# Performance work log

Hardware: AMD Instinct MI355X
Metric: run time of the kernel (lower is better)

The kernel has to match this reference:

```python
import jax, jax.numpy as jnp
import numpy as np


def setup_inputs() -> dict:
    key = jax.random.key(0)
    k1, k2, k3 = jax.random.split(key, 3)
    B, T, D = 2, 2048, 1024
    x = jax.random.normal(k1, (B, T, D), dtype=jnp.float32)
    w_qkv = jax.random.normal(k2, (3 * D, D), dtype=jnp.float32) * (D ** -0.5)
    w_out = jax.random.normal(k3, (D, D), dtype=jnp.float32) * (D ** -0.5)
    return {"x": x, "w_qkv": w_qkv, "w_out": w_out, "heads": 16}


def reference(x, w_qkv, w_out, heads):
    # SelfAttention forward: attention_type='sdp', position_mode='alibi', causal=True, eval mode.
    B, T, D = x.shape
    H = heads
    hd = D // H
    scale = hd ** -0.5

    # qkv projection: torch Linear -> x @ W^T
    qkv = (x @ w_qkv.T).reshape(B, T, 3, H, hd)
    qkv = jnp.transpose(qkv, (2, 0, 3, 1, 4))  # [3, B, H, T, hd]
    q, k, v = qkv[0], qkv[1], qkv[2]

    # ALiBi relative bias: slopes = 1 / 2^(h/H) for h = 1..H
    slopes = 1.0 / jnp.power(2.0, jnp.arange(1, H + 1, dtype=jnp.float32) / H)
    pos = jnp.arange(T, dtype=jnp.float32)
    rel = jnp.abs(pos[:, None] - pos[None, :])  # [T, T]
    bias = -slopes[None, :, None, None] * rel[None, None, :, :]  # [1, H, T, T]

    # scores + causal mask + softmax (manual path since position_bias is not None)
    scores = jnp.einsum('bhqd,bhkd->bhqk', q, k) * scale + bias
    causal_mask = jnp.triu(jnp.ones((T, T), dtype=bool), k=1)
    scores = jnp.where(causal_mask[None, None, :, :], -jnp.inf, scores)
    attn = jax.nn.softmax(scores, axis=-1)
    attn = jnp.where(jnp.isnan(attn), 1.0 / float(max(T, 1)), attn)

    out = jnp.einsum('bhqk,bhkd->bhqd', attn, v)  # [B, H, T, hd]
    out = jnp.transpose(out, (0, 2, 1, 3)).reshape(B, T, D)
    return out @ w_out.T
```

## Files before the change

kernel.cpp:

```cpp
#include <hip/hip_runtime.h>
#include <hip/hip_bf16.h>

typedef __attribute__((ext_vector_type(8))) short shortx8;
typedef __attribute__((ext_vector_type(4))) float floatx4;
typedef __attribute__((ext_vector_type(16))) float floatx16;
typedef __attribute__((ext_vector_type(4))) unsigned uintx4;
typedef __attribute__((ext_vector_type(2))) unsigned uintx2;

#define B_ 2
#define T_ 2048
#define D_ 1024
#define H_ 16
#define HD_ 64
#define SCALE 0.125f
#define QSCALE 0.18033688011112042f
#define SMAX2 23.083120654223414f
#define FULLH ((size_t)B_ * H_ * T_ * HD_)

#define GLDS16(g, l) __builtin_amdgcn_global_load_lds( \
    (__attribute__((address_space(1))) void*)(g), \
    (__attribute__((address_space(3))) void*)(l), 16, 0, 0)

__device__ __forceinline__ short f2bf(float f) {
    union { float f; unsigned u; } v; v.f = f;
    unsigned r = v.u + 0x7FFFu + ((v.u >> 16) & 1u);
    return (short)(r >> 16);
}

__device__ __forceinline__ unsigned pk2(float x, float y) {
    union { __hip_bfloat162 h; unsigned u; } t;
    t.h = __float22bfloat162_rn(make_float2(x, y));
    return t.u;
}

__device__ __forceinline__ shortx8 cvt8(floatx4 a, floatx4 b) {
    uintx4 r = { pk2(a[0], a[1]), pk2(a[2], a[3]), pk2(b[0], b[1]), pk2(b[2], b[3]) };
    return __builtin_bit_cast(shortx8, r);
}

__device__ __forceinline__ float ex2(float x) {
#if __has_builtin(__builtin_amdgcn_exp2f)
    return __builtin_amdgcn_exp2f(x);
#else
    return exp2f(x);
#endif
}

__global__ __launch_bounds__(256) void cvt_xw(const float* __restrict__ x,
                                              const float* __restrict__ wqkv,
                                              short* __restrict__ xbf,
                                              short* __restrict__ wbf) {
    int i = blockIdx.x * 256 + threadIdx.x;
    const float* src; short* dst; int o;
    if (i < 524288) { src = x; dst = xbf; o = i; }
    else            { src = wqkv; dst = wbf; o = i - 524288; }
    const floatx4* p = reinterpret_cast<const floatx4*>(src) + (size_t)o * 2;
    *(reinterpret_cast<shortx8*>(dst) + o) = cvt8(p[0], p[1]);
}

__global__ __launch_bounds__(256) void qkv_fast(const short* __restrict__ xbf,
                                                const short* __restrict__ wbf,
                                                short* __restrict__ qout,
                                                short* __restrict__ kv) {
    __shared__ __align__(16) short As[128 * 64];
    __shared__ __align__(16) short Bs[128 * 64];

    const int tid = threadIdx.x;
    const int wv = tid >> 6;
    const int l  = tid & 63;
    const int ln = l & 15;
    const int quad = l >> 4;
    const int rowb = quad << 2;
    const int wm = wv >> 1, wn = wv & 1;
    const int m0 = blockIdx.y * 128;
    const int n0g = blockIdx.x * 128;

    const int lr = l >> 3, lc = l & 7;
    const int gcol = (lc ^ lr) << 3;
    const short* agp = xbf + (size_t)(m0 + wv * 32 + lr) * D_ + gcol;
    const short* bgp = wbf + (size_t)(n0g + wv * 32 + lr) * D_ + gcol;
    short* aldsb = As + wv * 32 * 64;
    short* bldsb = Bs + wv * 32 * 64;

    floatx4 acc[4][4] = {};

    for (int k0 = 0; k0 < D_; k0 += 64) {
        __syncthreads();
#pragma unroll
        for (int c = 0; c < 4; ++c) {
            GLDS16(agp + (size_t)(c * 8) * D_ + k0, aldsb + c * 512);
            GLDS16(bgp + (size_t)(c * 8) * D_ + k0, bldsb + c * 512);
        }
        __syncthreads();

#pragma unroll
        for (int kk = 0; kk < 2; ++kk) {
            const int csw = (kk << 2) + quad;
            const int sw = (csw ^ (ln & 7)) << 3;
            shortx8 af[4], bf[4];
#pragma unroll
            for (int i = 0; i < 4; ++i)
                af[i] = *reinterpret_cast<const shortx8*>(&As[((wm * 64 + i * 16 + ln) << 6) + sw]);
#pragma unroll
            for (int j = 0; j < 4; ++j)
                bf[j] = *reinterpret_cast<const shortx8*>(&Bs[((wn * 64 + j * 16 + ln) << 6) + sw]);
#pragma unroll
            for (int i = 0; i < 4; ++i)
#pragma unroll
                for (int j = 0; j < 4; ++j)
                    acc[i][j] = __builtin_amdgcn_mfma_f32_16x16x32_bf16(af[i], bf[j], acc[i][j], 0, 0, 0);
        }
    }

    const int sel = n0g >> 10;
    const int bb = m0 >> 11;
    const int t0w = (m0 + wm * 64) & (T_ - 1);
    const int h = ((n0g + wn * 64) >> 6) & 15;

    if (sel < 2) {
        short* dst = (sel == 0) ? qout : kv;
        const float sc = (sel == 0) ? QSCALE : 1.0f;
        const size_t hb = (size_t)(bb * H_ + h) * T_;
#pragma unroll
        for (int i = 0; i < 4; ++i)
#pragma unroll
            for (int r = 0; r < 4; ++r) {
                int t = t0w + i * 16 + rowb + r;
#pragma unroll
                for (int j = 0; j < 4; ++j)
                    dst[(hb + t) * HD_ + j * 16 + ln] = f2bf(acc[i][j][r] * sc);
            }
    } else {
        __syncthreads();
        short* tb = (wv < 2) ? (As + wv * 4096) : (Bs + (wv - 2) * 4096);
        short* vhead = kv + FULLH + (size_t)(bb * H_ + h) * HD_ * T_;
        const int dl = l & 31, th = (l >> 5) << 5;
#pragma unroll
        for (int p = 0; p < 2; ++p) {
#pragma unroll
            for (int i = 0; i < 4; ++i)
#pragma unroll
                for (int jj = 0; jj < 2; ++jj) {
                    int j = 2 * p + jj;
#pragma unroll
                    for (int r = 0; r < 4; ++r)
                        tb[(jj * 16 + ln) * 72 + i * 16 + rowb + r] = f2bf(acc[i][j][r]);
                }
            short* vd = vhead + (size_t)(p * 32 + dl) * T_ + t0w + th;
#pragma unroll
            for (int seg = 0; seg < 4; ++seg)
                *reinterpret_cast<shortx8*>(vd + seg * 8) =
                    *reinterpret_cast<const shortx8*>(&tb[dl * 72 + th + seg * 8]);
        }
    }
}

__global__ __launch_bounds__(256) void out_fast(const short* __restrict__ Abf,
                                                const short* __restrict__ wbf,
                                                float* __restrict__ out) {
    __shared__ __align__(16) short As[128 * 64];
    __shared__ __align__(16) short Bs[128 * 64];

    const int tid = threadIdx.x;
    const int wv = tid >> 6;
    const int l  = tid & 63;
    const int ln = l & 15;
    const int quad = l >> 4;
    const int rowb = quad << 2;
    const int wm = wv >> 1, wn = wv & 1;
    const int m0 = blockIdx.y * 128;
    const int n0g = blockIdx.x * 128;

    const int lr = l >> 3, lc = l & 7;
    const int gcol = (lc ^ lr) << 3;
    const short* bgp = wbf + (size_t)(n0g + wv * 32 + lr) * D_ + gcol;
    short* aldsb = As + wv * 32 * 64;
    short* bldsb = Bs + wv * 32 * 64;

    size_t abase[4];
#pragma unroll
    for (int c = 0; c < 4; ++c) {
        int m = m0 + wv * 32 + c * 8 + lr;
        int bb2 = m >> 11, t = m & (T_ - 1);
        abase[c] = ((size_t)(bb2 * H_) * T_ + t) * HD_ + gcol;
    }

    floatx4 acc[4][4] = {};

    for (int k0 = 0; k0 < D_; k0 += 64) {
        const size_t hoff = (size_t)(k0 >> 6) * T_ * HD_;
        __syncthreads();
#pragma unroll
        for (int c = 0; c < 4; ++c) {
            GLDS16(Abf + abase[c] + hoff, aldsb + c * 512);
            GLDS16(bgp + (size_t)(c * 8) * D_ + k0, bldsb + c * 512);
        }
        __syncthreads();

#pragma unroll
        for (int kk = 0; kk < 2; ++kk) {
            const int csw = (kk << 2) + quad;
            const int sw = (csw ^ (ln & 7)) << 3;
            shortx8 af[4], bf[4];
#pragma unroll
            for (int i = 0; i < 4; ++i)
                af[i] = *reinterpret_cast<const shortx8*>(&As[((wm * 64 + i * 16 + ln) << 6) + sw]);
#pragma unroll
            for (int j = 0; j < 4; ++j)
                bf[j] = *reinterpret_cast<const shortx8*>(&Bs[((wn * 64 + j * 16 + ln) << 6) + sw]);
#pragma unroll
            for (int i = 0; i < 4; ++i)
#pragma unroll
                for (int j = 0; j < 4; ++j)
                    acc[i][j] = __builtin_amdgcn_mfma_f32_16x16x32_bf16(af[i], bf[j], acc[i][j], 0, 0, 0);
        }
    }

#pragma unroll
    for (int i = 0; i < 4; ++i)
#pragma unroll
        for (int r = 0; r < 4; ++r) {
            int m = m0 + wm * 64 + i * 16 + rowb + r;
#pragma unroll
            for (int j = 0; j < 4; ++j)
                out[(size_t)m * D_ + n0g + wn * 64 + j * 16 + ln] = acc[i][j][r];
        }
}

__global__ __launch_bounds__(128, 2) void attn(const short* __restrict__ qws,
                                               const short* __restrict__ kv,
                                               short* ao,
                                               const float* __restrict__ wout,
                                               short* __restrict__ wobf) {
    if (blockIdx.x >= 1024) {
        int i = (blockIdx.x - 1024) * 128 + threadIdx.x;
        const floatx4* p = reinterpret_cast<const floatx4*>(wout) + (size_t)i * 2;
        *(reinterpret_cast<shortx8*>(wobf) + i) = cvt8(p[0], p[1]);
        return;
    }

    __shared__ __align__(16) short Ks[64][72];
    __shared__ __align__(16) short Vt[64][72];

    const int tid = threadIdx.x;
    const int wv = tid >> 6;
    const int l  = tid & 63;
    const int ql = l & 31;
    const int hi = l >> 5;

    const int id  = blockIdx.x;
    const int xcd = id & 7;
    const int u2  = (id >> 3) & 3;
    const int rr  = (id >> 5) & 7;
    const int tt  = id >> 8;
    const int bh  = xcd * 4 + u2;
    const int qblk = (tt == 0) ? 31 - rr : (tt == 1) ? rr : (tt == 2) ? 23 - rr : 8 + rr;
    const int h = bh & 15, b = bh >> 4;

    const float slope2 = 1.4426950408889634f * exp2f(-(float)(h + 1) * 0.0625f);
    const size_t koff = (size_t)(b * H_ + h) * T_ * HD_;
    const int q0w = qblk * 64 + wv * 32;

    shortx8 qf[4];
#pragma unroll
    for (int ds = 0; ds < 4; ++ds)
        qf[ds] = *reinterpret_cast<const shortx8*>(&qws[koff + (size_t)(q0w + ql) * HD_ + ds * 16 + hi * 8]);

    const float cbase = slope2 * (float)(4 * hi - (q0w + ql)) - SMAX2;
    float rb[16];
#pragma unroll
    for (int g = 0; g < 16; ++g)
        rb[g] = cbase + slope2 * (float)((g & 3) + 8 * (g >> 2));
    const float s32 = slope2 * 32.0f;

    const int sr = tid >> 1;
    const int sc = (tid & 1) << 5;
    const short* kbase = kv + koff;
    const short* vbase = kv + FULLH + koff;
    shortx8 kR[4], vR[4];
    auto FETCH = [&](int kb) {
        const short* kp = kbase + (((size_t)(kb * 64 + sr)) << 6) + sc;
        const short* vp = vbase + (size_t)sr * T_ + kb * 64 + sc;
#pragma unroll
        for (int s = 0; s < 4; ++s) {
            kR[s] = *reinterpret_cast<const shortx8*>(kp + 8 * s);
            vR[s] = *reinterpret_cast<const shortx8*>(vp + 8 * s);
        }
    };

    floatx16 oacc0 = {}, oacc1 = {}, lsum = {};
    const shortx8 ones = {16256, 16256, 16256, 16256, 16256, 16256, 16256, 16256};
    const int qlh = ql - 4 * hi;

    FETCH(0);
    for (int kb = 0; kb <= qblk; ++kb) {
        __syncthreads();
#pragma unroll
        for (int s = 0; s < 4; ++s) {
            *reinterpret_cast<shortx8*>(&Ks[sr][sc + 8 * s]) = kR[s];
            *reinterpret_cast<shortx8*>(&Vt[sr][sc + 8 * s]) = vR[s];
        }
        __syncthreads();
        if (kb < qblk) FETCH(kb + 1);

        const bool diag = (kb == qblk);
        const float tb = slope2 * (float)(kb * 64);

#pragma unroll
        for (int nc = 0; nc < 2; ++nc) {
            const bool act = !diag || (nc == 0) || (wv == 1);
            if (!act) continue;
            const bool part = diag && (nc == wv);

            floatx16 s = {};
#pragma unroll
            for (int ds = 0; ds < 4; ++ds) {
                shortx8 kf = *reinterpret_cast<const shortx8*>(&Ks[nc * 32 + ql][ds * 16 + hi * 8]);
                s = __builtin_amdgcn_mfma_f32_32x32x16_bf16(kf, qf[ds], s, 0, 0, 0);
            }

            const float tnc = tb + (nc ? s32 : 0.0f);
            float p[16];
#pragma unroll
            for (int g = 0; g < 16; ++g) {
                float e = ex2(s[g] + rb[g] + tnc);
                if (part) {
                    const int kc = (g & 3) + 8 * (g >> 2);
                    e = (kc <= qlh) ? e : 0.0f;
                }
                p[g] = e;
            }

            unsigned cv[4][2];
#pragma unroll
            for (int g = 0; g < 4; ++g) {
                cv[g][0] = pk2(p[4 * g + 0], p[4 * g + 1]);
                cv[g][1] = pk2(p[4 * g + 2], p[4 * g + 3]);
            }

            __builtin_amdgcn_s_setprio(1);
#pragma unroll
            for (int kh = 0; kh < 2; ++kh) {
                unsigned w0 = cv[2 * kh][0], w2 = cv[2 * kh + 1][0];
                unsigned w1 = cv[2 * kh][1], w3 = cv[2 * kh + 1][1];
                asm volatile("v_permlane32_swap_b32 %0, %1" : "+v"(w0), "+v"(w2));
                asm volatile("v_permlane32_swap_b32 %0, %1" : "+v"(w1), "+v"(w3));
                uintx4 uu = {w0, w1, w2, w3};
                shortx8 apv = __builtin_bit_cast(shortx8, uu);
                const int ks = nc * 2 + kh;
                lsum = __builtin_amdgcn_mfma_f32_32x32x16_bf16(apv, ones, lsum, 0, 0, 0);
                shortx8 vf0 = *reinterpret_cast<const shortx8*>(&Vt[ql][ks * 16 + hi * 8]);
                oacc0 = __builtin_amdgcn_mfma_f32_32x32x16_bf16(apv, vf0, oacc0, 0, 0, 0);
                shortx8 vf1 = *reinterpret_cast<const shortx8*>(&Vt[32 + ql][ks * 16 + hi * 8]);
                oacc1 = __builtin_amdgcn_mfma_f32_32x32x16_bf16(apv, vf1, oacc1, 0, 0, 0);
            }
            __builtin_amdgcn_s_setprio(0);
        }
    }

#pragma unroll
    for (int g = 0; g < 16; ++g) {
        const int qrow = (g & 3) + 8 * (g >> 2) + 4 * hi;
        const float inv = 1.0f / lsum[g];
        const size_t ob = koff + (size_t)(q0w + qrow) * HD_ + ql;
        ao[ob]      = f2bf(oacc0[g] * inv);
        ao[ob + 32] = f2bf(oacc1[g] * inv);
    }
}

__global__ __launch_bounds__(256) void qkv_slow(const float* __restrict__ x,
                                                const float* __restrict__ wqkv,
                                                short* __restrict__ qout,
                                                short* __restrict__ kv) {
    __shared__ __align__(16) short As[64][72];
    __shared__ __align__(16) short Bs[64][72];
    const int tid = threadIdx.x;
    const int wv = tid >> 6, l = tid & 63, ln = l & 15, quad = l >> 4, qd = quad << 3;
    const int m0 = blockIdx.y * 64;
    const int sel = blockIdx.x >> 4, h = blockIdx.x & 15;
    const int nrow = sel * D_ + h * HD_;
    const int sr0 = tid >> 3, sc0 = (tid & 7) << 3, sr1 = sr0 + 32;
    floatx4 fa[4], fb[4];
    auto FETCH = [&](int k0) {
        const float* ap = &x[(size_t)(m0 + sr0) * D_ + k0 + sc0];
        fa[0] = *reinterpret_cast<const floatx4*>(ap);
        fa[1] = *reinterpret_cast<const floatx4*>(ap + 4);
        ap += (size_t)32 * D_;
        fa[2] = *reinterpret_cast<const floatx4*>(ap);
        fa[3] = *reinterpret_cast<const floatx4*>(ap + 4);
        const float* bp = &wqkv[(size_t)(nrow + sr0) * D_ + k0 + sc0];
        fb[0] = *reinterpret_cast<const floatx4*>(bp);
        fb[1] = *reinterpret_cast<const floatx4*>(bp + 4);
        bp += (size_t)32 * D_;
        fb[2] = *reinterpret_cast<const floatx4*>(bp);
        fb[3] = *reinterpret_cast<const floatx4*>(bp + 4);
    };
    floatx4 acc[4] = {};
    FETCH(0);
    for (int k0 = 0; k0 < D_; k0 += 64) {
        __syncthreads();
        *reinterpret_cast<shortx8*>(&As[sr0][sc0]) = cvt8(fa[0], fa[1]);
        *reinterpret_cast<shortx8*>(&As[sr1][sc0]) = cvt8(fa[2], fa[3]);
        *reinterpret_cast<shortx8*>(&Bs[sr0][sc0]) = cvt8(fb[0], fb[1]);
        *reinterpret_cast<shortx8*>(&Bs[sr1][sc0]) = cvt8(fb[2], fb[3]);
        __syncthreads();
        if (k0 + 64 < D_) FETCH(k0 + 64);
        const int mr = (wv << 4) + ln;
#pragma unroll
        for (int kk = 0; kk < 2; ++kk) {
            shortx8 a = *reinterpret_cast<const shortx8*>(&As[mr][kk * 32 + qd]);
#pragma unroll
            for (int nc = 0; nc < 4; ++nc) {
                shortx8 bq = *reinterpret_cast<const shortx8*>(&Bs[nc * 16 + ln][kk * 32 + qd]);
                acc[nc] = __builtin_amdgcn_mfma_f32_16x16x32_bf16(a, bq, acc[nc], 0, 0, 0);
            }
        }
    }
    const int bb = m0 >> 11, t0 = m0 & (T_ - 1);
    if (sel < 2) {
        short* dst = (sel == 0) ? qout : kv;
        const float sc = (sel == 0) ? QSCALE : 1.0f;
#pragma unroll
        for (int r = 0; r < 4; ++r) {
            int t = t0 + (wv << 4) + (quad << 2) + r;
#pragma unroll
            for (int nc = 0; nc < 4; ++nc)
                dst[((size_t)(bb * H_ + h) * T_ + t) * HD_ + nc * 16 + ln] = f2bf(acc[nc][r] * sc);
        }
    } else {
        __syncthreads();
#pragma unroll
        for (int r = 0; r < 4; ++r)
#pragma unroll
            for (int nc = 0; nc < 4; ++nc)
                As[nc * 16 + ln][(wv << 4) + (quad << 2) + r] = f2bf(acc[nc][r]);
        __syncthreads();
        const int d = tid >> 2, tseg = (tid & 3) << 4;
        short* vdst = kv + FULLH + ((size_t)(bb * H_ + h) * HD_ + d) * T_ + t0 + tseg;
        *reinterpret_cast<shortx8*>(vdst)     = *reinterpret_cast<const shortx8*>(&As[d][tseg]);
        *reinterpret_cast<shortx8*>(vdst + 8) = *reinterpret_cast<const shortx8*>(&As[d][tseg + 8]);
    }
}

__global__ __launch_bounds__(256) void out_slow(const short* __restrict__ A,
                                                const float* __restrict__ W,
                                                float* __restrict__ out) {
    __shared__ __align__(16) short As[64][72];
    __shared__ __align__(16) short Bs[64][72];
    const int tid = threadIdx.x;
    const int wv = tid >> 6, l = tid & 63, ln = l & 15, quad = l >> 4, qd = quad << 3;
    const int m0 = blockIdx.y * 64, n0 = blockIdx.x * 64;
    const int sr0 = tid >> 3, sc0 = (tid & 7) << 3, sr1 = sr0 + 32;
    shortx8 sa0, sa1;
    floatx4 fb[4];
    auto FETCH = [&](int k0) {
        const int h = k0 >> 6;
        int m = m0 + sr0;
        int bb = m >> 11, t = m & (T_ - 1);
        sa0 = *reinterpret_cast<const shortx8*>(A + ((size_t)(bb * H_ + h) * T_ + t) * HD_ + sc0);
        m = m0 + sr1; bb = m >> 11; t = m & (T_ - 1);
        sa1 = *reinterpret_cast<const shortx8*>(A + ((size_t)(bb * H_ + h) * T_ + t) * HD_ + sc0);
        const float* bp = &W[(size_t)(n0 + sr0) * D_ + k0 + sc0];
        fb[0] = *reinterpret_cast<const floatx4*>(bp);
        fb[1] = *reinterpret_cast<const floatx4*>(bp + 4);
        bp += (size_t)32 * D_;
        fb[2] = *reinterpret_cast<const floatx4*>(bp);
        fb[3] = *reinterpret_cast<const floatx4*>(bp + 4);
    };
    floatx4 acc[4] = {};
    FETCH(0);
    for (int k0 = 0; k0 < D_; k0 += 64) {
        __syncthreads();
        *reinterpret_cast<shortx8*>(&As[sr0][sc0]) = sa0;
        *reinterpret_cast<shortx8*>(&As[sr1][sc0]) = sa1;
        *reinterpret_cast<shortx8*>(&Bs[sr0][sc0]) = cvt8(fb[0], fb[1]);
        *reinterpret_cast<shortx8*>(&Bs[sr1][sc0]) = cvt8(fb[2], fb[3]);
        __syncthreads();
        if (k0 + 64 < D_) FETCH(k0 + 64);
        const int mr = (wv << 4) + ln;
#pragma unroll
        for (int kk = 0; kk < 2; ++kk) {
            shortx8 a = *reinterpret_cast<const shortx8*>(&As[mr][kk * 32 + qd]);
#pragma unroll
            for (int nc = 0; nc < 4; ++nc) {
                shortx8 bq = *reinterpret_cast<const shortx8*>(&Bs[nc * 16 + ln][kk * 32 + qd]);
                acc[nc] = __builtin_amdgcn_mfma_f32_16x16x32_bf16(a, bq, acc[nc], 0, 0, 0);
            }
        }
    }
#pragma unroll
    for (int r = 0; r < 4; ++r) {
        int m = m0 + (wv << 4) + (quad << 2) + r;
#pragma unroll
        for (int nc = 0; nc < 4; ++nc)
            out[(size_t)m * D_ + n0 + nc * 16 + ln] = acc[nc][r];
    }
}

extern "C" void kernel_launch(void* const* d_in, const int* in_sizes, int n_in,
                              void* d_out, int out_size, void* d_ws, size_t ws_size,
                              hipStream_t stream) {
    const float* x    = (const float*)d_in[0];
    const float* wqkv = (const float*)d_in[1];
    const float* wout = (const float*)d_in[2];

    short* kvbuf = (short*)d_out;
    float* out   = (float*)d_out;

    if (ws_size >= 23068672ULL) {
        short* xbf  = (short*)d_ws;
        short* wbf  = xbf + 4 * 1024 * 1024;
        short* qws  = xbf + 7 * 1024 * 1024;
        short* wobf = xbf;

        cvt_xw<<<3584, 256, 0, stream>>>(x, wqkv, xbf, wbf);
        qkv_fast<<<dim3(24, 32), 256, 0, stream>>>(xbf, wbf, qws, kvbuf);
        attn<<<dim3(2048), 128, 0, stream>>>(qws, kvbuf, qws, wout, wobf);
        out_fast<<<dim3(8, 32), 256, 0, stream>>>(qws, wobf, out);
    } else {
        short* qws = (short*)d_ws;
        qkv_slow<<<dim3(48, 64), 256, 0, stream>>>(x, wqkv, qws, kvbuf);
        attn<<<dim3(1024), 128, 0, stream>>>(qws, kvbuf, qws, nullptr, nullptr);
        out_slow<<<dim3(16, 64), 256, 0, stream>>>(qws, wout, out);
    }
}
```

Measured before the change: 182.0 us.

## Restructure attention into single-wave blocks loading K/V directly to registers

Each attention block is now one 64-lane wave that handles a pair of 32-row query groups (g and 63-g) to balance causal work. K and V are read straight from global memory into registers with a double-buffered prefetch, so there is no LDS staging and no __syncthreads. The wout conversion tail blocks are adjusted to the smaller block size. The cost is larger register use, uncoalesced strided global reads for V, and no K/V sharing between waves through LDS, which raises global and L2 traffic.

Measured after the change: 206.0 us. +13.2%, slower.

```diff
diff --git a/kernel.cpp b/kernel.cpp
--- a/kernel.cpp
+++ b/kernel.cpp
@@ -227,39 +227,17 @@
         }
 }
 
-__global__ __launch_bounds__(128, 2) void attn(const short* __restrict__ qws,
-                                               const short* __restrict__ kv,
-                                               short* ao,
-                                               const float* __restrict__ wout,
-                                               short* __restrict__ wobf) {
-    if (blockIdx.x >= 1024) {
-        int i = (blockIdx.x - 1024) * 128 + threadIdx.x;
-        const floatx4* p = reinterpret_cast<const floatx4*>(wout) + (size_t)i * 2;
-        *(reinterpret_cast<shortx8*>(wobf) + i) = cvt8(p[0], p[1]);
-        return;
-    }
-
-    __shared__ __align__(16) short Ks[64][72];
-    __shared__ __align__(16) short Vt[64][72];
-
-    const int tid = threadIdx.x;
-    const int wv = tid >> 6;
-    const int l  = tid & 63;
-    const int ql = l & 31;
-    const int hi = l >> 5;
-
-    const int id  = blockIdx.x;
-    const int xcd = id & 7;
-    const int u2  = (id >> 3) & 3;
-    const int rr  = (id >> 5) & 7;
-    const int tt  = id >> 8;
-    const int bh  = xcd * 4 + u2;
-    const int qblk = (tt == 0) ? 31 - rr : (tt == 1) ? rr : (tt == 2) ? 23 - rr : 8 + rr;
-    const int h = bh & 15, b = bh >> 4;
-
-    const float slope2 = 1.4426950408889634f * exp2f(-(float)(h + 1) * 0.0625f);
-    const size_t koff = (size_t)(b * H_ + h) * T_ * HD_;
-    const int q0w = qblk * 64 + wv * 32;
+__device__ __forceinline__ void attn_group(int g, int ql, int hi, float slope2,
+                                           size_t koff,
+                                           const short* __restrict__ qws,
+                                           const short* __restrict__ kbase,
+                                           const short* __restrict__ vbase,
+                                           short* __restrict__ ao) {
+    const int q0w = g * 32;
+    const int e = (g >> 1) + 1;
+    const int parity = g & 1;
+    const int qlh = ql - 4 * hi;
+    const float s32 = slope2 * 32.0f;
 
     shortx8 qf[4];
 #pragma unroll
@@ -269,75 +247,60 @@
     const float cbase = slope2 * (float)(4 * hi - (q0w + ql)) - SMAX2;
     float rb[16];
 #pragma unroll
-    for (int g = 0; g < 16; ++g)
-        rb[g] = cbase + slope2 * (float)((g & 3) + 8 * (g >> 2));
-    const float s32 = slope2 * 32.0f;
-
-    const int sr = tid >> 1;
-    const int sc = (tid & 1) << 5;
-    const short* kbase = kv + koff;
-    const short* vbase = kv + FULLH + koff;
-    shortx8 kR[4], vR[4];
-    auto FETCH = [&](int kb) {
-        const short* kp = kbase + (((size_t)(kb * 64 + sr)) << 6) + sc;
-        const short* vp = vbase + (size_t)sr * T_ + kb * 64 + sc;
-#pragma unroll
-        for (int s = 0; s < 4; ++s) {
-            kR[s] = *reinterpret_cast<const shortx8*>(kp + 8 * s);
-            vR[s] = *reinterpret_cast<const shortx8*>(vp + 8 * s);
-        }
+    for (int t = 0; t < 16; ++t)
+        rb[t] = cbase + slope2 * (float)((t & 3) + 8 * (t >> 2));
+
+    floatx16 o0 = {}, o1 = {}, ls = {};
+    const shortx8 ones = {16256, 16256, 16256, 16256, 16256, 16256, 16256, 16256};
+
+    const short* kq  = kbase + ql * HD_ + hi * 8;
+    const short* vq0 = vbase + (size_t)ql * T_ + hi * 8;
+    const short* vq1 = vbase + (size_t)(32 + ql) * T_ + hi * 8;
+
+    shortx8 kA[2][4], kB[2][4], vf[2][4];
+
+    auto LK = [&](int kb, shortx8 (&dst)[2][4]) {
+#pragma unroll
+        for (int nc = 0; nc < 2; ++nc)
+#pragma unroll
+            for (int ds = 0; ds < 4; ++ds)
+                dst[nc][ds] = *reinterpret_cast<const shortx8*>(kq + (kb * 64 + nc * 32) * HD_ + ds * 16);
     };
-
-    floatx16 oacc0 = {}, oacc1 = {}, lsum = {};
-    const shortx8 ones = {16256, 16256, 16256, 16256, 16256, 16256, 16256, 16256};
-    const int qlh = ql - 4 * hi;
-
-    FETCH(0);
-    for (int kb = 0; kb <= qblk; ++kb) {
-        __syncthreads();
-#pragma unroll
-        for (int s = 0; s < 4; ++s) {
-            *reinterpret_cast<shortx8*>(&Ks[sr][sc + 8 * s]) = kR[s];
-            *reinterpret_cast<shortx8*>(&Vt[sr][sc + 8 * s]) = vR[s];
-        }
-        __syncthreads();
-        if (kb < qblk) FETCH(kb + 1);
-
-        const bool diag = (kb == qblk);
+    auto LV = [&](int kb) {
+#pragma unroll
+        for (int ks = 0; ks < 4; ++ks) {
+            vf[0][ks] = *reinterpret_cast<const shortx8*>(vq0 + kb * 64 + ks * 16);
+            vf[1][ks] = *reinterpret_cast<const shortx8*>(vq1 + kb * 64 + ks * 16);
+        }
+    };
+    auto COMP = [&](const shortx8 (&kc)[2][4], int kb) {
+        const bool last = (kb == e - 1);
         const float tb = slope2 * (float)(kb * 64);
-
 #pragma unroll
         for (int nc = 0; nc < 2; ++nc) {
-            const bool act = !diag || (nc == 0) || (wv == 1);
-            if (!act) continue;
-            const bool part = diag && (nc == wv);
-
+            if (last && nc > parity) continue;
+            const bool part = last && (nc == parity);
             floatx16 s = {};
 #pragma unroll
-            for (int ds = 0; ds < 4; ++ds) {
-                shortx8 kf = *reinterpret_cast<const shortx8*>(&Ks[nc * 32 + ql][ds * 16 + hi * 8]);
-                s = __builtin_amdgcn_mfma_f32_32x32x16_bf16(kf, qf[ds], s, 0, 0, 0);
-            }
-
+            for (int ds = 0; ds < 4; ++ds)
+                s = __builtin_amdgcn_mfma_f32_32x32x16_bf16(kc[nc][ds], qf[ds], s, 0, 0, 0);
             const float tnc = tb + (nc ? s32 : 0.0f);
             float p[16];
 #pragma unroll
-            for (int g = 0; g < 16; ++g) {
-                float e = ex2(s[g] + rb[g] + tnc);
+            for (int t = 0; t < 16; ++t) {
+                float ev = ex2(s[t] + (rb[t] + tnc));
                 if (part) {
-                    const int kc = (g & 3) + 8 * (g >> 2);
-                    e = (kc <= qlh) ? e : 0.0f;
+                    const int kc2 = (t & 3) + 8 * (t >> 2);
+                    ev = (kc2 <= qlh) ? ev : 0.0f;
                 }
-                p[g] = e;
+                p[t] = ev;
             }
-
             unsigned cv[4][2];
 #pragma unroll
-            for (int g = 0; g < 4; ++g) {
-                cv[g][0] = pk2(p[4 * g + 0], p[4 * g + 1]);
-                cv[g][1] = pk2(p[4 * g + 2], p[4 * g + 3]);
+            for (int t = 0; t < 4; ++t) {
+                cv[t][0] = pk2(p[4 * t + 0], p[4 * t + 1]);
+                cv[t][1] = pk2(p[4 * t + 2], p[4 * t + 3]);
             }
-
             __builtin_amdgcn_s_setprio(1);
 #pragma unroll
             for (int kh = 0; kh < 2; ++kh) {
@@ -348,24 +311,64 @@
                 uintx4 uu = {w0, w1, w2, w3};
                 shortx8 apv = __builtin_bit_cast(shortx8, uu);
                 const int ks = nc * 2 + kh;
-                lsum = __builtin_amdgcn_mfma_f32_32x32x16_bf16(apv, ones, lsum, 0, 0, 0);
-                shortx8 vf0 = *reinterpret_cast<const shortx8*>(&Vt[ql][ks * 16 + hi * 8]);
-                oacc0 = __builtin_amdgcn_mfma_f32_32x32x16_bf16(apv, vf0, oacc0, 0, 0, 0);
-                shortx8 vf1 = *reinterpret_cast<const shortx8*>(&Vt[32 + ql][ks * 16 + hi * 8]);
-                oacc1 = __builtin_amdgcn_mfma_f32_32x32x16_bf16(apv, vf1, oacc1, 0, 0, 0);
+                ls = __builtin_amdgcn_mfma_f32_32x32x16_bf16(apv, ones, ls, 0, 0, 0);
+                o0 = __builtin_amdgcn_mfma_f32_32x32x16_bf16(apv, vf[0][ks], o0, 0, 0, 0);
+                o1 = __builtin_amdgcn_mfma_f32_32x32x16_bf16(apv, vf[1][ks], o1, 0, 0, 0);
             }
             __builtin_amdgcn_s_setprio(0);
         }
-    }
-
-#pragma unroll
-    for (int g = 0; g < 16; ++g) {
-        const int qrow = (g & 3) + 8 * (g >> 2) + 4 * hi;
-        const float inv = 1.0f / lsum[g];
+    };
+
+    LK(0, kA);
+    int kb = 0;
+    for (;;) {
+        LV(kb);
+        if (kb + 1 < e) LK(kb + 1, kB);
+        COMP(kA, kb);
+        ++kb; if (kb == e) break;
+        LV(kb);
+        if (kb + 1 < e) LK(kb + 1, kA);
+        COMP(kB, kb);
+        ++kb; if (kb == e) break;
+    }
+
+#pragma unroll
+    for (int t = 0; t < 16; ++t) {
+        const int qrow = (t & 3) + 8 * (t >> 2) + 4 * hi;
+        const float inv = 1.0f / ls[t];
         const size_t ob = koff + (size_t)(q0w + qrow) * HD_ + ql;
-        ao[ob]      = f2bf(oacc0[g] * inv);
-        ao[ob + 32] = f2bf(oacc1[g] * inv);
-    }
+        ao[ob]      = f2bf(o0[t] * inv);
+        ao[ob + 32] = f2bf(o1[t] * inv);
+    }
+}
+
+__global__ __launch_bounds__(64, 1) void attn(const short* __restrict__ qws,
+                                              const short* __restrict__ kv,
+                                              short* ao,
+                                              const float* __restrict__ wout,
+                                              short* __restrict__ wobf) {
+    if (blockIdx.x >= 1024) {
+        int i = (blockIdx.x - 1024) * 64 + threadIdx.x;
+        const floatx4* p = reinterpret_cast<const floatx4*>(wout) + (size_t)i * 2;
+        *(reinterpret_cast<shortx8*>(wobf) + i) = cvt8(p[0], p[1]);
+        return;
+    }
+    const int l  = threadIdx.x;
+    const int ql = l & 31, hi = l >> 5;
+    const int id  = blockIdx.x;
+    const int xcd = id & 7;
+    const int u2  = (id >> 3) & 3;
+    const int pr  = id >> 5;
+    const int bh  = xcd * 4 + u2;
+    const int h = bh & 15, b = bh >> 4;
+
+    const float slope2 = 1.4426950408889634f * exp2f(-(float)(h + 1) * 0.0625f);
+    const size_t koff = (size_t)(b * H_ + h) * T_ * HD_;
+    const short* kbase = kv + koff;
+    const short* vbase = kv + FULLH + koff;
+
+    attn_group(63 - pr, ql, hi, slope2, koff, qws, kbase, vbase, ao);
+    attn_group(pr,      ql, hi, slope2, koff, qws, kbase, vbase, ao);
 }
 
 __global__ __launch_bounds__(256) void qkv_slow(const float* __restrict__ x,
@@ -515,12 +518,12 @@
 
         cvt_xw<<<3584, 256, 0, stream>>>(x, wqkv, xbf, wbf);
         qkv_fast<<<dim3(24, 32), 256, 0, stream>>>(xbf, wbf, qws, kvbuf);
-        attn<<<dim3(2048), 128, 0, stream>>>(qws, kvbuf, qws, wout, wobf);
+        attn<<<dim3(3072), 64, 0, stream>>>(qws, kvbuf, qws, wout, wobf);
         out_fast<<<dim3(8, 32), 256, 0, stream>>>(qws, wobf, out);
     } else {
         short* qws = (short*)d_ws;
         qkv_slow<<<dim3(48, 64), 256, 0, stream>>>(x, wqkv, qws, kvbuf);
-        attn<<<dim3(1024), 128, 0, stream>>>(qws, kvbuf, qws, nullptr, nullptr);
+        attn<<<dim3(1024), 64, 0, stream>>>(qws, kvbuf, qws, nullptr, nullptr);
         out_slow<<<dim3(16, 64), 256, 0, stream>>>(qws, wout, out);
     }
 }
```

## Pair complementary causal query blocks per workgroup and double-buffer K/V in LDS

Applied to the files above, without the earlier changes.

Each attention workgroup now processes two query blocks (qblk and 31-qblk) in sequence, so every block does the same amount of causal work and only half as many blocks are launched. The K/V LDS tiles are double-buffered, so staging the next tile overlaps compute on the current one, with one barrier per iteration instead of two. The cost is twice the LDS per block, which may lower occupancy, and fewer blocks in the grid, which reduces parallelism and latency hiding.

New measurement: 191.2 us. +5.0%, slower.

```diff
diff --git a/kernel.cpp b/kernel.cpp
--- a/kernel.cpp
+++ b/kernel.cpp
@@ -232,15 +232,15 @@
                                                short* ao,
                                                const float* __restrict__ wout,
                                                short* __restrict__ wobf) {
-    if (blockIdx.x >= 1024) {
-        int i = (blockIdx.x - 1024) * 128 + threadIdx.x;
+    if (blockIdx.x >= 512) {
+        int i = (blockIdx.x - 512) * 128 + threadIdx.x;
         const floatx4* p = reinterpret_cast<const floatx4*>(wout) + (size_t)i * 2;
         *(reinterpret_cast<shortx8*>(wobf) + i) = cvt8(p[0], p[1]);
         return;
     }
 
-    __shared__ __align__(16) short Ks[64][72];
-    __shared__ __align__(16) short Vt[64][72];
+    __shared__ __align__(16) short Ks[2][64][72];
+    __shared__ __align__(16) short Vt[2][64][72];
 
     const int tid = threadIdx.x;
     const int wv = tid >> 6;
@@ -251,26 +251,13 @@
     const int id  = blockIdx.x;
     const int xcd = id & 7;
     const int u2  = (id >> 3) & 3;
-    const int rr  = (id >> 5) & 7;
-    const int tt  = id >> 8;
+    const int pr  = id >> 5;
     const int bh  = xcd * 4 + u2;
-    const int qblk = (tt == 0) ? 31 - rr : (tt == 1) ? rr : (tt == 2) ? 23 - rr : 8 + rr;
     const int h = bh & 15, b = bh >> 4;
 
     const float slope2 = 1.4426950408889634f * exp2f(-(float)(h + 1) * 0.0625f);
     const size_t koff = (size_t)(b * H_ + h) * T_ * HD_;
-    const int q0w = qblk * 64 + wv * 32;
-
-    shortx8 qf[4];
-#pragma unroll
-    for (int ds = 0; ds < 4; ++ds)
-        qf[ds] = *reinterpret_cast<const shortx8*>(&qws[koff + (size_t)(q0w + ql) * HD_ + ds * 16 + hi * 8]);
-
-    const float cbase = slope2 * (float)(4 * hi - (q0w + ql)) - SMAX2;
-    float rb[16];
-#pragma unroll
-    for (int g = 0; g < 16; ++g)
-        rb[g] = cbase + slope2 * (float)((g & 3) + 8 * (g >> 2));
+    const int qlh = ql - 4 * hi;
     const float s32 = slope2 * 32.0f;
 
     const int sr = tid >> 1;
@@ -287,84 +274,110 @@
             vR[s] = *reinterpret_cast<const shortx8*>(vp + 8 * s);
         }
     };
-
-    floatx16 oacc0 = {}, oacc1 = {}, lsum = {};
+    auto STAGE = [&](int bi) {
+#pragma unroll
+        for (int s = 0; s < 4; ++s) {
+            *reinterpret_cast<shortx8*>(&Ks[bi][sr][sc + 8 * s]) = kR[s];
+            *reinterpret_cast<shortx8*>(&Vt[bi][sr][sc + 8 * s]) = vR[s];
+        }
+    };
+
     const shortx8 ones = {16256, 16256, 16256, 16256, 16256, 16256, 16256, 16256};
-    const int qlh = ql - 4 * hi;
-
-    FETCH(0);
-    for (int kb = 0; kb <= qblk; ++kb) {
-        __syncthreads();
-#pragma unroll
-        for (int s = 0; s < 4; ++s) {
-            *reinterpret_cast<shortx8*>(&Ks[sr][sc + 8 * s]) = kR[s];
-            *reinterpret_cast<shortx8*>(&Vt[sr][sc + 8 * s]) = vR[s];
-        }
-        __syncthreads();
-        if (kb < qblk) FETCH(kb + 1);
-
-        const bool diag = (kb == qblk);
-        const float tb = slope2 * (float)(kb * 64);
-
-#pragma unroll
-        for (int nc = 0; nc < 2; ++nc) {
-            const bool act = !diag || (nc == 0) || (wv == 1);
-            if (!act) continue;
-            const bool part = diag && (nc == wv);
-
-            floatx16 s = {};
-#pragma unroll
-            for (int ds = 0; ds < 4; ++ds) {
-                shortx8 kf = *reinterpret_cast<const shortx8*>(&Ks[nc * 32 + ql][ds * 16 + hi * 8]);
-                s = __builtin_amdgcn_mfma_f32_32x32x16_bf16(kf, qf[ds], s, 0, 0, 0);
+
+    for (int ph = 0; ph < 2; ++ph) {
+        const int qblk = ph ? pr : 31 - pr;
+        const int e = qblk + 1;
+        const int q0w = qblk * 64 + wv * 32;
+
+        shortx8 qf[4];
+#pragma unroll
+        for (int ds = 0; ds < 4; ++ds)
+            qf[ds] = *reinterpret_cast<const shortx8*>(&qws[koff + (size_t)(q0w + ql) * HD_ + ds * 16 + hi * 8]);
+
+        const float cbase = slope2 * (float)(4 * hi - (q0w + ql)) - SMAX2;
+        float rb[16];
+#pragma unroll
+        for (int t = 0; t < 16; ++t)
+            rb[t] = cbase + slope2 * (float)((t & 3) + 8 * (t >> 2));
+
+        floatx16 o0 = {}, o1 = {}, ls = {};
+
+        FETCH(0);
+        STAGE(0);
+        if (e > 1) FETCH(1);
+        __syncthreads();
+
+        for (int kb = 0; kb < e; ++kb) {
+            const int cur = kb & 1;
+            if (kb + 1 < e) {
+                STAGE(cur ^ 1);
+                if (kb + 2 < e) FETCH(kb + 2);
             }
 
-            const float tnc = tb + (nc ? s32 : 0.0f);
-            float p[16];
-#pragma unroll
-            for (int g = 0; g < 16; ++g) {
-                float e = ex2(s[g] + rb[g] + tnc);
-                if (part) {
-                    const int kc = (g & 3) + 8 * (g >> 2);
-                    e = (kc <= qlh) ? e : 0.0f;
+            const bool diag = (kb == qblk);
+            const float tb = slope2 * (float)(kb * 64);
+
+#pragma unroll
+            for (int nc = 0; nc < 2; ++nc) {
+                const bool act = !diag || (nc == 0) || (wv == 1);
+                if (!act) continue;
+                const bool part = diag && (nc == wv);
+
+                floatx16 sacc = {};
+#pragma unroll
+                for (int ds = 0; ds < 4; ++ds) {
+                    shortx8 kf = *reinterpret_cast<const shortx8*>(&Ks[cur][nc * 32 + ql][ds * 16 + hi * 8]);
+                    sacc = __builtin_amdgcn_mfma_f32_32x32x16_bf16(kf, qf[ds], sacc, 0, 0, 0);
                 }
-                p[g] = e;
+
+                const float tnc = tb + (nc ? s32 : 0.0f);
+                float p[16];
+#pragma unroll
+                for (int t = 0; t < 16; ++t) {
+                    float ev = ex2(sacc[t] + (rb[t] + tnc));
+                    if (part) {
+                        const int kc2 = (t & 3) + 8 * (t >> 2);
+                        ev = (kc2 <= qlh) ? ev : 0.0f;
+                    }
+                    p[t] = ev;
+                }
+
+                unsigned cv[4][2];
+#pragma unroll
+                for (int t = 0; t < 4; ++t) {
+                    cv[t][0] = pk2(p[4 * t + 0], p[4 * t + 1]);
+                    cv[t][1] = pk2(p[4 * t + 2], p[4 * t + 3]);
+                }
+
+                __builtin_amdgcn_s_setprio(1);
+#pragma unroll
+                for (int kh = 0; kh < 2; ++kh) {
+                    unsigned w0 = cv[2 * kh][0], w2 = cv[2 * kh + 1][0];
+                    unsigned w1 = cv[2 * kh][1], w3 = cv[2 * kh + 1][1];
+                    asm volatile("v_permlane32_swap_b32 %0, %1" : "+v"(w0), "+v"(w2));
+                    asm volatile("v_permlane32_swap_b32 %0, %1" : "+v"(w1), "+v"(w3));
+                    uintx4 uu = {w0, w1, w2, w3};
+                    shortx8 apv = __builtin_bit_cast(shortx8, uu);
+                    const int ks = nc * 2 + kh;
+                    ls = __builtin_amdgcn_mfma_f32_32x32x16_bf16(apv, ones, ls, 0, 0, 0);
+                    shortx8 vf0 = *reinterpret_cast<const shortx8*>(&Vt[cur][ql][ks * 16 + hi * 8]);
+                    o0 = __builtin_amdgcn_mfma_f32_32x32x16_bf16(apv, vf0, o0, 0, 0, 0);
+                    shortx8 vf1 = *reinterpret_cast<const shortx8*>(&Vt[cur][32 + ql][ks * 16 + hi * 8]);
+                    o1 = __builtin_amdgcn_mfma_f32_32x32x16_bf16(apv, vf1, o1, 0, 0, 0);
+                }
+                __builtin_amdgcn_s_setprio(0);
             }
-
-            unsigned cv[4][2];
-#pragma unroll
-            for (int g = 0; g < 4; ++g) {
-                cv[g][0] = pk2(p[4 * g + 0], p[4 * g + 1]);
-                cv[g][1] = pk2(p[4 * g + 2], p[4 * g + 3]);
-            }
-
-            __builtin_amdgcn_s_setprio(1);
-#pragma unroll
-            for (int kh = 0; kh < 2; ++kh) {
-                unsigned w0 = cv[2 * kh][0], w2 = cv[2 * kh + 1][0];
-                unsigned w1 = cv[2 * kh][1], w3 = cv[2 * kh + 1][1];
-                asm volatile("v_permlane32_swap_b32 %0, %1" : "+v"(w0), "+v"(w2));
-                asm volatile("v_permlane32_swap_b32 %0, %1" : "+v"(w1), "+v"(w3));
-                uintx4 uu = {w0, w1, w2, w3};
-                shortx8 apv = __builtin_bit_cast(shortx8, uu);
-                const int ks = nc * 2 + kh;
-                lsum = __builtin_amdgcn_mfma_f32_32x32x16_bf16(apv, ones, lsum, 0, 0, 0);
-                shortx8 vf0 = *reinterpret_cast<const shortx8*>(&Vt[ql][ks * 16 + hi * 8]);
-                oacc0 = __builtin_amdgcn_mfma_f32_32x32x16_bf16(apv, vf0, oacc0, 0, 0, 0);
-                shortx8 vf1 = *reinterpret_cast<const shortx8*>(&Vt[32 + ql][ks * 16 + hi * 8]);
-                oacc1 = __builtin_amdgcn_mfma_f32_32x32x16_bf16(apv, vf1, oacc1, 0, 0, 0);
-            }
-            __builtin_amdgcn_s_setprio(0);
-        }
-    }
-
-#pragma unroll
-    for (int g = 0; g < 16; ++g) {
-        const int qrow = (g & 3) + 8 * (g >> 2) + 4 * hi;
-        const float inv = 1.0f / lsum[g];
-        const size_t ob = koff + (size_t)(q0w + qrow) * HD_ + ql;
-        ao[ob]      = f2bf(oacc0[g] * inv);
-        ao[ob + 32] = f2bf(oacc1[g] * inv);
+            __syncthreads();
+        }
+
+#pragma unroll
+        for (int t = 0; t < 16; ++t) {
+            const int qrow = (t & 3) + 8 * (t >> 2) + 4 * hi;
+            const float inv = 1.0f / ls[t];
+            const size_t ob = koff + (size_t)(q0w + qrow) * HD_ + ql;
+            ao[ob]      = f2bf(o0[t] * inv);
+            ao[ob + 32] = f2bf(o1[t] * inv);
+        }
     }
 }
 
@@ -515,12 +528,12 @@
 
         cvt_xw<<<3584, 256, 0, stream>>>(x, wqkv, xbf, wbf);
         qkv_fast<<<dim3(24, 32), 256, 0, stream>>>(xbf, wbf, qws, kvbuf);
-        attn<<<dim3(2048), 128, 0, stream>>>(qws, kvbuf, qws, wout, wobf);
+        attn<<<dim3(1536), 128, 0, stream>>>(qws, kvbuf, qws, wout, wobf);
         out_fast<<<dim3(8, 32), 256, 0, stream>>>(qws, wobf, out);
     } else {
         short* qws = (short*)d_ws;
         qkv_slow<<<dim3(48, 64), 256, 0, stream>>>(x, wqkv, qws, kvbuf);
-        attn<<<dim3(1024), 128, 0, stream>>>(qws, kvbuf, qws, nullptr, nullptr);
+        attn<<<dim3(512), 128, 0, stream>>>(qws, kvbuf, qws, nullptr, nullptr);
         out_slow<<<dim3(16, 64), 256, 0, stream>>>(qws, wout, out);
     }
 }
```

## Load K/V tiles directly into LDS with XOR-swizzled unpadded layout

Applied to the files above, without the earlier changes.

Replaces the register-staged K/V prefetch (global→VGPR→LDS) with direct global_load_lds transfers into an unpadded, XOR-swizzled LDS layout, and updates the fragment reads to match the swizzle. This removes the staging registers and LDS store instructions and avoids bank conflicts without padding. In exchange, the next tile is no longer prefetched during compute, so global load latency may be exposed at each iteration's barrier.

After: 184.8 us. Within noise of the previous version (+1.5%).

```diff
diff --git a/kernel.cpp b/kernel.cpp
--- a/kernel.cpp
+++ b/kernel.cpp
@@ -239,8 +239,8 @@
         return;
     }
 
-    __shared__ __align__(16) short Ks[64][72];
-    __shared__ __align__(16) short Vt[64][72];
+    __shared__ __align__(16) short Ks[64 * 64];
+    __shared__ __align__(16) short Vt[64 * 64];
 
     const int tid = threadIdx.x;
     const int wv = tid >> 6;
@@ -273,35 +273,27 @@
         rb[g] = cbase + slope2 * (float)((g & 3) + 8 * (g >> 2));
     const float s32 = slope2 * 32.0f;
 
-    const int sr = tid >> 1;
-    const int sc = (tid & 1) << 5;
-    const short* kbase = kv + koff;
-    const short* vbase = kv + FULLH + koff;
-    shortx8 kR[4], vR[4];
-    auto FETCH = [&](int kb) {
-        const short* kp = kbase + (((size_t)(kb * 64 + sr)) << 6) + sc;
-        const short* vp = vbase + (size_t)sr * T_ + kb * 64 + sc;
-#pragma unroll
-        for (int s = 0; s < 4; ++s) {
-            kR[s] = *reinterpret_cast<const shortx8*>(kp + 8 * s);
-            vR[s] = *reinterpret_cast<const shortx8*>(vp + 8 * s);
-        }
-    };
-
-    floatx16 oacc0 = {}, oacc1 = {}, lsum = {};
+    const int lr = l >> 3, lc = l & 7;
+    const int gcol = (lc ^ lr) << 3;
+    const short* kgp = kv + koff + (size_t)(wv * 32 + lr) * HD_ + gcol;
+    const short* vgp = kv + FULLH + koff + (size_t)(wv * 32 + lr) * T_ + gcol;
+    short* klds = Ks + wv * 32 * 64;
+    short* vlds = Vt + wv * 32 * 64;
+
+    const int qs7 = ql & 7;
+
+    floatx16 o0 = {}, o1 = {}, ls = {};
     const shortx8 ones = {16256, 16256, 16256, 16256, 16256, 16256, 16256, 16256};
     const int qlh = ql - 4 * hi;
 
-    FETCH(0);
     for (int kb = 0; kb <= qblk; ++kb) {
         __syncthreads();
 #pragma unroll
-        for (int s = 0; s < 4; ++s) {
-            *reinterpret_cast<shortx8*>(&Ks[sr][sc + 8 * s]) = kR[s];
-            *reinterpret_cast<shortx8*>(&Vt[sr][sc + 8 * s]) = vR[s];
-        }
-        __syncthreads();
-        if (kb < qblk) FETCH(kb + 1);
+        for (int c = 0; c < 4; ++c) {
+            GLDS16(kgp + (size_t)(kb * 64 + c * 8) * HD_, klds + c * 512);
+            GLDS16(vgp + (size_t)(c * 8) * T_ + kb * 64, vlds + c * 512);
+        }
+        __syncthreads();
 
         const bool diag = (kb == qblk);
         const float tb = slope2 * (float)(kb * 64);
@@ -312,23 +304,24 @@
             if (!act) continue;
             const bool part = diag && (nc == wv);
 
-            floatx16 s = {};
+            floatx16 sacc = {};
 #pragma unroll
             for (int ds = 0; ds < 4; ++ds) {
-                shortx8 kf = *reinterpret_cast<const shortx8*>(&Ks[nc * 32 + ql][ds * 16 + hi * 8]);
-                s = __builtin_amdgcn_mfma_f32_32x32x16_bf16(kf, qf[ds], s, 0, 0, 0);
+                const int kcol = ((ds * 2 + hi) ^ qs7) << 3;
+                shortx8 kf = *reinterpret_cast<const shortx8*>(&Ks[((nc * 32 + ql) << 6) + kcol]);
+                sacc = __builtin_amdgcn_mfma_f32_32x32x16_bf16(kf, qf[ds], sacc, 0, 0, 0);
             }
 
             const float tnc = tb + (nc ? s32 : 0.0f);
             float p[16];
 #pragma unroll
             for (int g = 0; g < 16; ++g) {
-                float e = ex2(s[g] + rb[g] + tnc);
+                float ev = ex2(sacc[g] + (rb[g] + tnc));
                 if (part) {
-                    const int kc = (g & 3) + 8 * (g >> 2);
-                    e = (kc <= qlh) ? e : 0.0f;
+                    const int kc2 = (g & 3) + 8 * (g >> 2);
+                    ev = (kc2 <= qlh) ? ev : 0.0f;
                 }
-                p[g] = e;
+                p[g] = ev;
             }
 
             unsigned cv[4][2];
@@ -348,11 +341,12 @@
                 uintx4 uu = {w0, w1, w2, w3};
                 shortx8 apv = __builtin_bit_cast(shortx8, uu);
                 const int ks = nc * 2 + kh;
-                lsum = __builtin_amdgcn_mfma_f32_32x32x16_bf16(apv, ones, lsum, 0, 0, 0);
-                shortx8 vf0 = *reinterpret_cast<const shortx8*>(&Vt[ql][ks * 16 + hi * 8]);
-                oacc0 = __builtin_amdgcn_mfma_f32_32x32x16_bf16(apv, vf0, oacc0, 0, 0, 0);
-                shortx8 vf1 = *reinterpret_cast<const shortx8*>(&Vt[32 + ql][ks * 16 + hi * 8]);
-                oacc1 = __builtin_amdgcn_mfma_f32_32x32x16_bf16(apv, vf1, oacc1, 0, 0, 0);
+                const int vcol = ((ks * 2 + hi) ^ qs7) << 3;
+                ls = __builtin_amdgcn_mfma_f32_32x32x16_bf16(apv, ones, ls, 0, 0, 0);
+                shortx8 vf0 = *reinterpret_cast<const shortx8*>(&Vt[(ql << 6) + vcol]);
+                o0 = __builtin_amdgcn_mfma_f32_32x32x16_bf16(apv, vf0, o0, 0, 0, 0);
+                shortx8 vf1 = *reinterpret_cast<const shortx8*>(&Vt[((32 + ql) << 6) + vcol]);
+                o1 = __builtin_amdgcn_mfma_f32_32x32x16_bf16(apv, vf1, o1, 0, 0, 0);
             }
             __builtin_amdgcn_s_setprio(0);
         }
@@ -361,10 +355,10 @@
 #pragma unroll
     for (int g = 0; g < 16; ++g) {
         const int qrow = (g & 3) + 8 * (g >> 2) + 4 * hi;
-        const float inv = 1.0f / lsum[g];
+        const float inv = 1.0f / ls[g];
         const size_t ob = koff + (size_t)(q0w + qrow) * HD_ + ql;
-        ao[ob]      = f2bf(oacc0[g] * inv);
-        ao[ob + 32] = f2bf(oacc1[g] * inv);
+        ao[ob]      = f2bf(o0[g] * inv);
+        ao[ob + 32] = f2bf(o1[g] * inv);
     }
 }
 
```
